# Performance work log

Measured on AMD Instinct MI355X. Metric: run time of the kernel, lower is better.

Reference implementation:

```python
import jax, jax.numpy as jnp
import numpy as np

K = 32          # kneighbors
HEADS = 4       # Anchor_selfattention head_num
EPS = 1e-5      # BatchNorm eps


def bn(x, gamma, beta):
    # training-mode BatchNorm1d on channel-last tensor [B, M, C]:
    # stats over batch+spatial dims per channel, biased variance (torch behavior)
    m = jnp.mean(x, axis=(0, 1), keepdims=True)
    v = jnp.var(x, axis=(0, 1), keepdims=True)
    return gamma * (x - m) * jax.lax.rsqrt(v + EPS) + beta


def setup_inputs() -> dict:
    B, NA, NP, C, NRAW = 32, 4, 16384, 256, 32768
    key = jax.random.key(0)
    ks = jax.random.split(key, 12)
    s = 0.02
    return {
        "a_points": jax.random.normal(ks[0], (B, NA, 3), jnp.float32),
        "sa_x": jax.random.normal(ks[1], (B, NP, C), jnp.float32),
        "sa_xyz": jax.random.normal(ks[2], (B, NP, 3), jnp.float32),
        "xyz_raw": jax.random.normal(ks[3], (B, NRAW, 3), jnp.float32),
        # global_layer: Conv1d(3->C, bias=False) + BN(C)
        "g_W": jax.random.normal(ks[4], (C, 3), jnp.float32) * s,
        "g_gamma": jnp.ones((C,), jnp.float32),
        "g_beta": jnp.zeros((C,), jnp.float32),
        # attention: to_qkv Linear(C -> 3C, bias=False)
        "qkv_W": jax.random.normal(ks[5], (3 * C, C), jnp.float32) * s,
        # pos_embedding: Conv1d(3->C) + BN(C)
        "pos_W": jax.random.normal(ks[6], (C, 3), jnp.float32) * s,
        "pos_b": jnp.zeros((C,), jnp.float32),
        "pos_gamma": jnp.ones((C,), jnp.float32),
        "pos_beta": jnp.zeros((C,), jnp.float32),
        # res: Conv1d(C->C) + BN(C)
        "res_W": jax.random.normal(ks[7], (C, C), jnp.float32) * s,
        "res_b": jnp.zeros((C,), jnp.float32),
        "res_gamma": jnp.ones((C,), jnp.float32),
        "res_beta": jnp.zeros((C,), jnp.float32),
        # prob_head: Conv1d(2C -> 9, bias=False) + BN(9)
        "prob_W": jax.random.normal(ks[8], (9, 2 * C), jnp.float32) * s,
        "prob_gamma": jnp.ones((9,), jnp.float32),
        "prob_beta": jnp.zeros((9,), jnp.float32),
    }


def reference(a_points, sa_x, sa_xyz, xyz_raw,
              g_W, g_gamma, g_beta,
              qkv_W,
              pos_W, pos_b, pos_gamma, pos_beta,
              res_W, res_b, res_gamma, res_beta,
              prob_W, prob_gamma, prob_beta):
    B, NA, _ = a_points.shape
    C = sa_x.shape[-1]
    hd = C // HEADS

    # ---- knn_point: squared distances anchor->points, smallest-K indices ----
    # dist[b, a, n] = |a_points[b,a] - sa_xyz[b,n]|^2
    d = (-2.0 * jnp.einsum("bac,bnc->ban", a_points, sa_xyz)
         + jnp.sum(a_points ** 2, -1)[:, :, None]
         + jnp.sum(sa_xyz ** 2, -1)[:, None, :])
    _, idx = jax.lax.top_k(-d, K)                      # [B, NA, K]

    # ---- index_points gather + max-pool over neighbors ----
    local = jnp.take_along_axis(sa_x[:, None, :, :], idx[..., None], axis=2)  # [B,NA,K,C]
    local_feat = jnp.max(local, axis=2)                # [B, NA, C]

    # ---- Anchor self-attention ----
    gc = jnp.mean(a_points, axis=1, keepdims=True)
    rel = a_points - gc                                # [B, NA, 3]
    pos = bn(rel @ pos_W.T + pos_b, pos_gamma, pos_beta)   # [B, NA, C]

    qkv = local_feat @ qkv_W.T                         # [B, NA, 3C]
    q, k, v = jnp.split(qkv, 3, axis=-1)
    q, k, v = q + pos, k + pos, v + pos
    q = q.reshape(B, NA, HEADS, hd)
    k = k.reshape(B, NA, HEADS, hd)
    v = v.reshape(B, NA, HEADS, hd)
    attn = jnp.einsum("bmhd,bnhd->bhmn", q, k) / np.sqrt(hd).astype(np.float32)
    attn = jax.nn.softmax(attn, axis=-1)
    av = jnp.einsum("bhmn,bnhd->bmhd", attn, v).reshape(B, NA, C)
    res = bn(av @ res_W.T + res_b, res_gamma, res_beta)

    local_feat = local_feat + res                      # [B, NA, C]

    # ---- global branch ----
    gfeat = bn(a_points @ g_W.T, g_gamma, g_beta)      # [B, NA, C]
    gmax = jnp.max(gfeat, axis=1, keepdims=True)       # [B, 1, C]
    feat = jnp.concatenate(
        [local_feat, jnp.broadcast_to(gmax, (B, NA, C))], axis=-1)  # [B, NA, 2C]

    prob = bn(feat @ prob_W.T, prob_gamma, prob_beta)  # [B, NA, 9]
    return prob
```

## Files before the change

### kernel.cpp

```cpp
#include <hip/hip_runtime.h>
#include <math.h>

#define NPTS 16384
#define HALF 8192
#define NB   32
#define NA   4
#define NC   256
#define KNN  32
#define NROW 128
#define CAP  1024

#define OFF_LF      0
#define OFF_QKV     32768
#define OFF_RESLIN  131072
#define OFF_POSLIN  163840
#define OFF_POSST   196608
#define OFF_GLIN    197120
#define OFF_GST     229888
#define OFF_PROBLIN 230400
#define OFF_CAND    231552

__global__ __launch_bounds__(512) void knn_part_kernel(
    const float* __restrict__ a_points, const float* __restrict__ sa_xyz,
    uint2* __restrict__ cand)
{
  const int blk  = blockIdx.x;
  const int row  = blk >> 1;
  const int half = blk & 1;
  const int b    = row >> 2;
  const int t    = threadIdx.x;

  __shared__ float s_T;
  __shared__ int   s_m;
  __shared__ uint2 s_cand[CAP];
  float* smin = (float*)s_cand;

  const float ax = a_points[row*3 + 0];
  const float ay = a_points[row*3 + 1];
  const float az = a_points[row*3 + 2];
  const float* __restrict__ xyz = sa_xyz + (size_t)b * NPTS * 3 + (size_t)half * HALF * 3;

  float d[16];
#pragma unroll
  for (int j = 0; j < 16; ++j) {
    const int n = t + 512*j;
    const float dx = xyz[n*3+0] - ax;
    const float dy = xyz[n*3+1] - ay;
    const float dz = xyz[n*3+2] - az;
    d[j] = dx*dx + dy*dy + dz*dz;
  }
  float mn = d[0];
#pragma unroll
  for (int j = 1; j < 16; ++j) mn = fminf(mn, d[j]);
  if (t == 0) s_m = 0;
  smin[t] = mn;
  __syncthreads();

  if (t < 64) {
    unsigned v[8];
#pragma unroll
    for (int q = 0; q < 8; ++q) v[q] = __float_as_uint(smin[t + 64*q]);
    unsigned lo = 0u, hi = 0x7f7fffffu;
    while (lo < hi) {
      const unsigned mid = lo + ((hi - lo) >> 1);
      int cnt = 0;
#pragma unroll
      for (int q = 0; q < 8; ++q) cnt += (int)__popcll(__ballot(v[q] <= mid));
      if (cnt >= KNN) hi = mid; else lo = mid + 1;
    }
    if (t == 0) s_T = __uint_as_float(lo);
  }
  __syncthreads();
  const float T = s_T;

#pragma unroll
  for (int j = 0; j < 16; ++j) {
    if (d[j] <= T) {
      const int pos = atomicAdd(&s_m, 1);
      if (pos < CAP) s_cand[pos] = make_uint2(__float_as_uint(d[j]),
                                              (unsigned)(half*HALF + t + 512*j));
    }
  }
  __syncthreads();
  const int m = (s_m < CAP) ? s_m : CAP;

  for (int c2 = t; c2 < m; c2 += 512) {
    const uint2 me = s_cand[c2];
    int rank = 0;
    for (int j = 0; j < m; ++j) {
      const uint2 o = s_cand[j];
      rank += (o.x < me.x) || (o.x == me.x && o.y < me.y);
    }
    if (rank < KNN) cand[(size_t)blk*KNN + rank] = me;
  }
}

__global__ __launch_bounds__(256) void gather_kernel(
    const uint2* __restrict__ cand, const float* __restrict__ sa_x,
    float* __restrict__ lf)
{
  const int row = blockIdx.x;
  const int b   = row >> 2;
  const int t   = threadIdx.x;
  __shared__ uint2 s64[64];
  __shared__ int   s_top[KNN];
  if (t < 64) s64[t] = cand[(size_t)row*64 + t];
  __syncthreads();
  if (t < 64) {
    const uint2 me = s64[t];
    int rank = 0;
#pragma unroll
    for (int j = 0; j < 64; ++j) {
      const uint2 o = s64[j];
      rank += (o.x < me.x) || (o.x == me.x && o.y < me.y);
    }
    if (rank < KNN) s_top[rank] = (int)me.y;
  }
  __syncthreads();

  const float* __restrict__ xb = sa_x + (size_t)b * NPTS * NC;
  float acc = -3.0e38f;
#pragma unroll
  for (int r = 0; r < KNN; ++r)
    acc = fmaxf(acc, xb[(size_t)s_top[r] * NC + t]);
  lf[(size_t)row * NC + t] = acc;
}

__global__ __launch_bounds__(256) void lin1_kernel(
    const float* __restrict__ lf, const float* __restrict__ qkv_W,
    const float* __restrict__ a_points,
    const float* __restrict__ pos_W, const float* __restrict__ pos_b,
    const float* __restrict__ g_W,
    float* __restrict__ qkv, float* __restrict__ pos_lin, float* __restrict__ pos_stats,
    float* __restrict__ g_lin, float* __restrict__ g_stats)
{
  const int blk = blockIdx.x;
  if (blk < 96) {
    const int r0 = (blk / 12) * 16;
    const int o0 = (blk % 12) * 64;
    const int ot = threadIdx.x & 63;
    const int rt = threadIdx.x >> 6;
    const int o  = o0 + ot;
    const float* __restrict__ wrow = qkv_W + (size_t)o * NC;
    const float* __restrict__ l0p  = lf + (size_t)(r0 + rt*4) * NC;
    float acc0 = 0.f, acc1 = 0.f, acc2 = 0.f, acc3 = 0.f;
    for (int c = 0; c < NC; c += 4) {
      const float4 w4 = *(const float4*)(wrow + c);
      const float4 l0 = *(const float4*)(l0p + c);
      const float4 l1 = *(const float4*)(l0p + NC + c);
      const float4 l2 = *(const float4*)(l0p + 2*NC + c);
      const float4 l3 = *(const float4*)(l0p + 3*NC + c);
      acc0 = fmaf(l0.x,w4.x,acc0); acc0 = fmaf(l0.y,w4.y,acc0); acc0 = fmaf(l0.z,w4.z,acc0); acc0 = fmaf(l0.w,w4.w,acc0);
      acc1 = fmaf(l1.x,w4.x,acc1); acc1 = fmaf(l1.y,w4.y,acc1); acc1 = fmaf(l1.z,w4.z,acc1); acc1 = fmaf(l1.w,w4.w,acc1);
      acc2 = fmaf(l2.x,w4.x,acc2); acc2 = fmaf(l2.y,w4.y,acc2); acc2 = fmaf(l2.z,w4.z,acc2); acc2 = fmaf(l2.w,w4.w,acc2);
      acc3 = fmaf(l3.x,w4.x,acc3); acc3 = fmaf(l3.y,w4.y,acc3); acc3 = fmaf(l3.z,w4.z,acc3); acc3 = fmaf(l3.w,w4.w,acc3);
    }
    const int r = r0 + rt*4;
    qkv[(size_t)(r+0)*768 + o] = acc0;
    qkv[(size_t)(r+1)*768 + o] = acc1;
    qkv[(size_t)(r+2)*768 + o] = acc2;
    qkv[(size_t)(r+3)*768 + o] = acc3;
  } else if (blk == 96) {
    __shared__ float apts[NROW*3];
    for (int i = threadIdx.x; i < NROW*3; i += 256) apts[i] = a_points[i];
    __syncthreads();
    const int c = threadIdx.x;
    const float w0 = pos_W[c*3+0], w1 = pos_W[c*3+1], w2 = pos_W[c*3+2];
    const float bb = pos_b[c];
    float sum = 0.f, sumsq = 0.f;
    for (int b = 0; b < NB; ++b) {
      float gx=0.f, gy=0.f, gz=0.f;
#pragma unroll
      for (int a = 0; a < NA; ++a) {
        gx += apts[(b*NA+a)*3+0];
        gy += apts[(b*NA+a)*3+1];
        gz += apts[(b*NA+a)*3+2];
      }
      gx *= 0.25f; gy *= 0.25f; gz *= 0.25f;
#pragma unroll
      for (int a = 0; a < NA; ++a) {
        const float v = (apts[(b*NA+a)*3+0]-gx)*w0
                      + (apts[(b*NA+a)*3+1]-gy)*w1
                      + (apts[(b*NA+a)*3+2]-gz)*w2 + bb;
        pos_lin[(b*NA+a)*NC + c] = v;
        sum += v; sumsq += v*v;
      }
    }
    pos_stats[c] = sum; pos_stats[NC + c] = sumsq;
  } else {
    __shared__ float apts[NROW*3];
    for (int i = threadIdx.x; i < NROW*3; i += 256) apts[i] = a_points[i];
    __syncthreads();
    const int c = threadIdx.x;
    const float w0 = g_W[c*3+0], w1 = g_W[c*3+1], w2 = g_W[c*3+2];
    float sum = 0.f, sumsq = 0.f;
    for (int r = 0; r < NROW; ++r) {
      const float v = apts[r*3+0]*w0 + apts[r*3+1]*w1 + apts[r*3+2]*w2;
      g_lin[r*NC + c] = v;
      sum += v; sumsq += v*v;
    }
    g_stats[c] = sum; g_stats[NC + c] = sumsq;
  }
}

__global__ __launch_bounds__(256) void attn_kernel(
    const float* __restrict__ qkv, const float* __restrict__ pos_lin,
    const float* __restrict__ pos_stats,
    const float* __restrict__ pos_gamma, const float* __restrict__ pos_beta,
    const float* __restrict__ res_W, const float* __restrict__ res_b,
    float* __restrict__ res_lin)
{
  const int b = blockIdx.x;
  const int t = threadIdx.x;
  __shared__ float av_s[NA][NC];
  const int c = t;
  const float pmean = pos_stats[c] * (1.0f/NROW);
  const float pvar  = pos_stats[NC + c] * (1.0f/NROW) - pmean*pmean;
  const float prstd = 1.0f / sqrtf(pvar + 1e-5f);
  const float pga = pos_gamma[c], pbe = pos_beta[c];

  float q[NA], k[NA], vv[NA];
#pragma unroll
  for (int a = 0; a < NA; ++a) {
    const int row = b*NA + a;
    const float p = pga * (pos_lin[(size_t)row*NC + c] - pmean) * prstd + pbe;
    q[a]  = qkv[(size_t)row*768 +       c] + p;
    k[a]  = qkv[(size_t)row*768 + 256 + c] + p;
    vv[a] = qkv[(size_t)row*768 + 512 + c] + p;
  }
  float s[NA][NA];
#pragma unroll
  for (int m = 0; m < NA; ++m) {
#pragma unroll
    for (int n = 0; n < NA; ++n) {
      float p = q[m]*k[n];
#pragma unroll
      for (int off = 1; off < 64; off <<= 1) p += __shfl_xor(p, off);
      s[m][n] = p * 0.125f;
    }
  }
#pragma unroll
  for (int m = 0; m < NA; ++m) {
    const float mx = fmaxf(fmaxf(s[m][0], s[m][1]), fmaxf(s[m][2], s[m][3]));
    const float e0 = expf(s[m][0]-mx), e1 = expf(s[m][1]-mx);
    const float e2 = expf(s[m][2]-mx), e3 = expf(s[m][3]-mx);
    const float inv = 1.0f / (e0+e1+e2+e3);
    av_s[m][c] = (e0*vv[0] + e1*vv[1] + e2*vv[2] + e3*vv[3]) * inv;
  }
  __syncthreads();

  const float* __restrict__ wrow = res_W + (size_t)c * NC;
  float r0=0.f, r1=0.f, r2=0.f, r3=0.f;
  for (int cc = 0; cc < NC; cc += 4) {
    const float4 w4 = *(const float4*)(wrow + cc);
    const float4 v0 = *(const float4*)&av_s[0][cc];
    const float4 v1 = *(const float4*)&av_s[1][cc];
    const float4 v2 = *(const float4*)&av_s[2][cc];
    const float4 v3 = *(const float4*)&av_s[3][cc];
    r0 = fmaf(v0.x,w4.x,r0); r0 = fmaf(v0.y,w4.y,r0); r0 = fmaf(v0.z,w4.z,r0); r0 = fmaf(v0.w,w4.w,r0);
    r1 = fmaf(v1.x,w4.x,r1); r1 = fmaf(v1.y,w4.y,r1); r1 = fmaf(v1.z,w4.z,r1); r1 = fmaf(v1.w,w4.w,r1);
    r2 = fmaf(v2.x,w4.x,r2); r2 = fmaf(v2.y,w4.y,r2); r2 = fmaf(v2.z,w4.z,r2); r2 = fmaf(v2.w,w4.w,r2);
    r3 = fmaf(v3.x,w4.x,r3); r3 = fmaf(v3.y,w4.y,r3); r3 = fmaf(v3.z,w4.z,r3); r3 = fmaf(v3.w,w4.w,r3);
  }
  const float bias = res_b[c];
  res_lin[(size_t)(b*NA+0)*NC + c] = r0 + bias;
  res_lin[(size_t)(b*NA+1)*NC + c] = r1 + bias;
  res_lin[(size_t)(b*NA+2)*NC + c] = r2 + bias;
  res_lin[(size_t)(b*NA+3)*NC + c] = r3 + bias;
}

__global__ __launch_bounds__(256) void final_kernel(
    const float* __restrict__ lf, const float* __restrict__ res_lin,
    const float* __restrict__ res_gamma, const float* __restrict__ res_beta,
    const float* __restrict__ g_lin, const float* __restrict__ g_stats,
    const float* __restrict__ g_gamma, const float* __restrict__ g_beta,
    const float* __restrict__ prob_W,
    float* __restrict__ prob_lin)
{
  const int b = blockIdx.x;
  const int t = threadIdx.x;
  __shared__ float feat_s[NA][2 * NC];
  const int c = t;
  float rsum = 0.f, rss = 0.f;
  for (int row = 0; row < NROW; ++row) {
    const float v = res_lin[(size_t)row*NC + c];
    rsum += v; rss += v*v;
  }
  const float rmean = rsum * (1.0f/NROW);
  const float rvar  = rss * (1.0f/NROW) - rmean*rmean;
  const float rrstd = 1.0f / sqrtf(rvar + 1e-5f);
  const float rg = res_gamma[c], rb = res_beta[c];

  const float gmean = g_stats[c] * (1.0f/NROW);
  const float gvar  = g_stats[NC+c] * (1.0f/NROW) - gmean*gmean;
  const float grstd = 1.0f / sqrtf(gvar + 1e-5f);
  const float gg = g_gamma[c], gb = g_beta[c];

  float gm = -3.0e38f;
#pragma unroll
  for (int a = 0; a < NA; ++a) {
    const int row = b*NA + a;
    gm = fmaxf(gm, gg * (g_lin[(size_t)row*NC + c] - gmean) * grstd + gb);
  }
#pragma unroll
  for (int a = 0; a < NA; ++a) {
    const int row = b*NA + a;
    const float resv = rg * (res_lin[(size_t)row*NC + c] - rmean) * rrstd + rb;
    feat_s[a][c]      = lf[(size_t)row*NC + c] + resv;
    feat_s[a][NC + c] = gm;
  }
  __syncthreads();

  const int m = t >> 6, lane = t & 63;
  for (int j = 0; j < 9; ++j) {
    float p = 0.f;
#pragma unroll
    for (int k2 = 0; k2 < 8; ++k2) {
      const int cc = lane + 64*k2;
      p = fmaf(feat_s[m][cc], prob_W[j*2*NC + cc], p);
    }
#pragma unroll
    for (int off = 1; off < 64; off <<= 1) p += __shfl_xor(p, off);
    if (lane == 0) prob_lin[(b*NA+m)*9 + j] = p;
  }
}

__global__ __launch_bounds__(256) void out_kernel(
    const float* __restrict__ prob_lin,
    const float* __restrict__ prob_gamma, const float* __restrict__ prob_beta,
    float* __restrict__ out)
{
  const int t = threadIdx.x;
  __shared__ float pmn[9], prs[9];
  if (t < 9) {
    float s = 0.f, ss = 0.f;
    for (int i = 0; i < NROW; ++i) { const float v = prob_lin[i*9+t]; s += v; ss += v*v; }
    const float m  = s * (1.0f/NROW);
    const float va = ss * (1.0f/NROW) - m*m;
    pmn[t] = m; prs[t] = 1.0f / sqrtf(va + 1e-5f);
  }
  __syncthreads();
  for (int i = t; i < NROW*9; i += 256) {
    const int j = i % 9;
    out[i] = prob_gamma[j] * (prob_lin[i] - pmn[j]) * prs[j] + prob_beta[j];
  }
}

extern "C" void kernel_launch(void* const* d_in, const int* in_sizes, int n_in,
                              void* d_out, int out_size, void* d_ws, size_t ws_size,
                              hipStream_t stream) {
  const float* a_points  = (const float*)d_in[0];
  const float* sa_x      = (const float*)d_in[1];
  const float* sa_xyz    = (const float*)d_in[2];
  const float* g_W       = (const float*)d_in[4];
  const float* g_gamma   = (const float*)d_in[5];
  const float* g_beta    = (const float*)d_in[6];
  const float* qkv_W     = (const float*)d_in[7];
  const float* pos_W     = (const float*)d_in[8];
  const float* pos_b     = (const float*)d_in[9];
  const float* pos_gamma = (const float*)d_in[10];
  const float* pos_beta  = (const float*)d_in[11];
  const float* res_W     = (const float*)d_in[12];
  const float* res_b     = (const float*)d_in[13];
  const float* res_gamma = (const float*)d_in[14];
  const float* res_beta  = (const float*)d_in[15];
  const float* prob_W    = (const float*)d_in[16];
  const float* prob_gamma= (const float*)d_in[17];
  const float* prob_beta = (const float*)d_in[18];
  float* ws  = (float*)d_ws;
  float* out = (float*)d_out;

  knn_part_kernel<<<256, 512, 0, stream>>>(a_points, sa_xyz, (uint2*)(ws + OFF_CAND));
  gather_kernel<<<NROW, 256, 0, stream>>>((const uint2*)(ws + OFF_CAND), sa_x, ws + OFF_LF);
  lin1_kernel<<<98, 256, 0, stream>>>(ws + OFF_LF, qkv_W, a_points, pos_W, pos_b, g_W,
      ws + OFF_QKV, ws + OFF_POSLIN, ws + OFF_POSST, ws + OFF_GLIN, ws + OFF_GST);
  attn_kernel<<<NB, 256, 0, stream>>>(ws + OFF_QKV, ws + OFF_POSLIN, ws + OFF_POSST,
      pos_gamma, pos_beta, res_W, res_b, ws + OFF_RESLIN);
  final_kernel<<<NB, 256, 0, stream>>>(ws + OFF_LF, ws + OFF_RESLIN,
      res_gamma, res_beta, ws + OFF_GLIN, ws + OFF_GST, g_gamma, g_beta, prob_W,
      ws + OFF_PROBLIN);
  out_kernel<<<1, 256, 0, stream>>>(ws + OFF_PROBLIN, prob_gamma, prob_beta, out);
}
```

Before: 63.80 us.

## Fuse KNN, gather, QKV projection and output BN via last-block atomic counters

Merges knn, gather and lin1 kernels into one launch: the second half-block for each anchor row, detected through an atomic counter in workspace, merges candidates, gathers max features and computes that row's QKV projection. The pos and global linear parts run in two extra blocks. The output BatchNorm is folded into final_kernel using a last-block-done counter. This cuts three kernel launches and their inter-kernel gaps, at the cost of a less parallel QKV matmul (one row per block, weights reread per row) and counters that are never reset, relying on parity/modulo arithmetic across calls.

```diff
diff --git a/kernel.cpp b/kernel.cpp
--- a/kernel.cpp
+++ b/kernel.cpp
@@ -19,20 +19,76 @@
 #define OFF_GST     229888
 #define OFF_PROBLIN 230400
 #define OFF_CAND    231552
-
-__global__ __launch_bounds__(512) void knn_part_kernel(
+#define OFF_CNT     247936
+
+__global__ __launch_bounds__(512) void knn_fused_kernel(
     const float* __restrict__ a_points, const float* __restrict__ sa_xyz,
-    uint2* __restrict__ cand)
+    const float* __restrict__ sa_x, const float* __restrict__ qkv_W,
+    const float* __restrict__ pos_W, const float* __restrict__ pos_b,
+    const float* __restrict__ g_W,
+    uint2* __restrict__ cand, unsigned int* __restrict__ cnt,
+    float* __restrict__ lf, float* __restrict__ qkv,
+    float* __restrict__ pos_lin, float* __restrict__ pos_stats,
+    float* __restrict__ g_lin, float* __restrict__ g_stats)
 {
-  const int blk  = blockIdx.x;
-  const int row  = blk >> 1;
-  const int half = blk & 1;
+  const int blk = blockIdx.x;
+  const int t   = threadIdx.x;
+
+  if (blk < 2) {
+    __shared__ float apts[NROW * 3];
+    for (int i = t; i < NROW*3; i += 512) apts[i] = a_points[i];
+    __syncthreads();
+    if (t < NC) {
+      const int c = t;
+      if (blk == 0) {
+        const float w0 = pos_W[c*3+0], w1 = pos_W[c*3+1], w2 = pos_W[c*3+2];
+        const float bb = pos_b[c];
+        float sum = 0.f, sumsq = 0.f;
+        for (int b = 0; b < NB; ++b) {
+          float gx=0.f, gy=0.f, gz=0.f;
+#pragma unroll
+          for (int a = 0; a < NA; ++a) {
+            gx += apts[(b*NA+a)*3+0];
+            gy += apts[(b*NA+a)*3+1];
+            gz += apts[(b*NA+a)*3+2];
+          }
+          gx *= 0.25f; gy *= 0.25f; gz *= 0.25f;
+#pragma unroll
+          for (int a = 0; a < NA; ++a) {
+            const float v = (apts[(b*NA+a)*3+0]-gx)*w0
+                          + (apts[(b*NA+a)*3+1]-gy)*w1
+                          + (apts[(b*NA+a)*3+2]-gz)*w2 + bb;
+            pos_lin[(b*NA+a)*NC + c] = v;
+            sum += v; sumsq += v*v;
+          }
+        }
+        pos_stats[c] = sum; pos_stats[NC + c] = sumsq;
+      } else {
+        const float w0 = g_W[c*3+0], w1 = g_W[c*3+1], w2 = g_W[c*3+2];
+        float sum = 0.f, sumsq = 0.f;
+        for (int r = 0; r < NROW; ++r) {
+          const float v = apts[r*3+0]*w0 + apts[r*3+1]*w1 + apts[r*3+2]*w2;
+          g_lin[r*NC + c] = v;
+          sum += v; sumsq += v*v;
+        }
+        g_stats[c] = sum; g_stats[NC + c] = sumsq;
+      }
+    }
+    return;
+  }
+
+  const int row  = (blk - 2) >> 1;
+  const int half = (blk - 2) & 1;
   const int b    = row >> 2;
-  const int t    = threadIdx.x;
 
   __shared__ float s_T;
   __shared__ int   s_m;
+  __shared__ int   s_winflag;
   __shared__ uint2 s_cand[CAP];
+  __shared__ uint2 s64[64];
+  __shared__ int   s_top[KNN];
+  __shared__ float s_lf2[2][NC];
+  __shared__ float lf_s[NC];
   float* smin = (float*)s_cand;
 
   const float ax = a_points[row*3 + 0];
@@ -63,10 +119,10 @@
     unsigned lo = 0u, hi = 0x7f7fffffu;
     while (lo < hi) {
       const unsigned mid = lo + ((hi - lo) >> 1);
-      int cnt = 0;
-#pragma unroll
-      for (int q = 0; q < 8; ++q) cnt += (int)__popcll(__ballot(v[q] <= mid));
-      if (cnt >= KNN) hi = mid; else lo = mid + 1;
+      int cnt2 = 0;
+#pragma unroll
+      for (int q = 0; q < 8; ++q) cnt2 += (int)__popcll(__ballot(v[q] <= mid));
+      if (cnt2 >= KNN) hi = mid; else lo = mid + 1;
     }
     if (t == 0) s_T = __uint_as_float(lo);
   }
@@ -91,19 +147,19 @@
       const uint2 o = s_cand[j];
       rank += (o.x < me.x) || (o.x == me.x && o.y < me.y);
     }
-    if (rank < KNN) cand[(size_t)blk*KNN + rank] = me;
-  }
-}
-
-__global__ __launch_bounds__(256) void gather_kernel(
-    const uint2* __restrict__ cand, const float* __restrict__ sa_x,
-    float* __restrict__ lf)
-{
-  const int row = blockIdx.x;
-  const int b   = row >> 2;
-  const int t   = threadIdx.x;
-  __shared__ uint2 s64[64];
-  __shared__ int   s_top[KNN];
+    if (rank < KNN) cand[(size_t)row*64 + half*KNN + rank] = me;
+  }
+  __syncthreads();
+
+  if (t == 0) {
+    __threadfence();
+    const unsigned old = atomicAdd(&cnt[row], 1u);
+    s_winflag = (((old + 1u) & 1u) == 0u);
+  }
+  __syncthreads();
+  if (!s_winflag) return;
+  __threadfence();
+
   if (t < 64) s64[t] = cand[(size_t)row*64 + t];
   __syncthreads();
   if (t < 64) {
@@ -118,88 +174,41 @@
   }
   __syncthreads();
 
-  const float* __restrict__ xb = sa_x + (size_t)b * NPTS * NC;
-  float acc = -3.0e38f;
-#pragma unroll
-  for (int r = 0; r < KNN; ++r)
-    acc = fmaxf(acc, xb[(size_t)s_top[r] * NC + t]);
-  lf[(size_t)row * NC + t] = acc;
-}
-
-__global__ __launch_bounds__(256) void lin1_kernel(
-    const float* __restrict__ lf, const float* __restrict__ qkv_W,
-    const float* __restrict__ a_points,
-    const float* __restrict__ pos_W, const float* __restrict__ pos_b,
-    const float* __restrict__ g_W,
-    float* __restrict__ qkv, float* __restrict__ pos_lin, float* __restrict__ pos_stats,
-    float* __restrict__ g_lin, float* __restrict__ g_stats)
-{
-  const int blk = blockIdx.x;
-  if (blk < 96) {
-    const int r0 = (blk / 12) * 16;
-    const int o0 = (blk % 12) * 64;
-    const int ot = threadIdx.x & 63;
-    const int rt = threadIdx.x >> 6;
-    const int o  = o0 + ot;
-    const float* __restrict__ wrow = qkv_W + (size_t)o * NC;
-    const float* __restrict__ l0p  = lf + (size_t)(r0 + rt*4) * NC;
-    float acc0 = 0.f, acc1 = 0.f, acc2 = 0.f, acc3 = 0.f;
+  {
+    const int c = t & 255, h = t >> 8;
+    const float* __restrict__ xb = sa_x + (size_t)b * NPTS * NC;
+    float acc = -3.0e38f;
+    for (int r = h*16; r < h*16 + 16; ++r)
+      acc = fmaxf(acc, xb[(size_t)s_top[r] * NC + c]);
+    s_lf2[h][c] = acc;
+  }
+  __syncthreads();
+  if (t < NC) {
+    const float v = fmaxf(s_lf2[0][t], s_lf2[1][t]);
+    lf_s[t] = v;
+    lf[(size_t)row * NC + t] = v;
+  }
+  __syncthreads();
+
+  {
+    const float* __restrict__ w1 = qkv_W + (size_t)t * NC;
+    float a1 = 0.f;
     for (int c = 0; c < NC; c += 4) {
-      const float4 w4 = *(const float4*)(wrow + c);
-      const float4 l0 = *(const float4*)(l0p + c);
-      const float4 l1 = *(const float4*)(l0p + NC + c);
-      const float4 l2 = *(const float4*)(l0p + 2*NC + c);
-      const float4 l3 = *(const float4*)(l0p + 3*NC + c);
-      acc0 = fmaf(l0.x,w4.x,acc0); acc0 = fmaf(l0.y,w4.y,acc0); acc0 = fmaf(l0.z,w4.z,acc0); acc0 = fmaf(l0.w,w4.w,acc0);
-      acc1 = fmaf(l1.x,w4.x,acc1); acc1 = fmaf(l1.y,w4.y,acc1); acc1 = fmaf(l1.z,w4.z,acc1); acc1 = fmaf(l1.w,w4.w,acc1);
-      acc2 = fmaf(l2.x,w4.x,acc2); acc2 = fmaf(l2.y,w4.y,acc2); acc2 = fmaf(l2.z,w4.z,acc2); acc2 = fmaf(l2.w,w4.w,acc2);
-      acc3 = fmaf(l3.x,w4.x,acc3); acc3 = fmaf(l3.y,w4.y,acc3); acc3 = fmaf(l3.z,w4.z,acc3); acc3 = fmaf(l3.w,w4.w,acc3);
-    }
-    const int r = r0 + rt*4;
-    qkv[(size_t)(r+0)*768 + o] = acc0;
-    qkv[(size_t)(r+1)*768 + o] = acc1;
-    qkv[(size_t)(r+2)*768 + o] = acc2;
-    qkv[(size_t)(r+3)*768 + o] = acc3;
-  } else if (blk == 96) {
-    __shared__ float apts[NROW*3];
-    for (int i = threadIdx.x; i < NROW*3; i += 256) apts[i] = a_points[i];
-    __syncthreads();
-    const int c = threadIdx.x;
-    const float w0 = pos_W[c*3+0], w1 = pos_W[c*3+1], w2 = pos_W[c*3+2];
-    const float bb = pos_b[c];
-    float sum = 0.f, sumsq = 0.f;
-    for (int b = 0; b < NB; ++b) {
-      float gx=0.f, gy=0.f, gz=0.f;
-#pragma unroll
-      for (int a = 0; a < NA; ++a) {
-        gx += apts[(b*NA+a)*3+0];
-        gy += apts[(b*NA+a)*3+1];
-        gz += apts[(b*NA+a)*3+2];
+      const float4 l4 = *(const float4*)&lf_s[c];
+      const float4 w4 = *(const float4*)(w1 + c);
+      a1 = fmaf(l4.x,w4.x,a1); a1 = fmaf(l4.y,w4.y,a1); a1 = fmaf(l4.z,w4.z,a1); a1 = fmaf(l4.w,w4.w,a1);
+    }
+    qkv[(size_t)row*768 + t] = a1;
+    if (t < 256) {
+      const float* __restrict__ w2 = qkv_W + (size_t)(512 + t) * NC;
+      float a2 = 0.f;
+      for (int c = 0; c < NC; c += 4) {
+        const float4 l4 = *(const float4*)&lf_s[c];
+        const float4 w4 = *(const float4*)(w2 + c);
+        a2 = fmaf(l4.x,w4.x,a2); a2 = fmaf(l4.y,w4.y,a2); a2 = fmaf(l4.z,w4.z,a2); a2 = fmaf(l4.w,w4.w,a2);
       }
-      gx *= 0.25f; gy *= 0.25f; gz *= 0.25f;
-#pragma unroll
-      for (int a = 0; a < NA; ++a) {
-        const float v = (apts[(b*NA+a)*3+0]-gx)*w0
-                      + (apts[(b*NA+a)*3+1]-gy)*w1
-                      + (apts[(b*NA+a)*3+2]-gz)*w2 + bb;
-        pos_lin[(b*NA+a)*NC + c] = v;
-        sum += v; sumsq += v*v;
-      }
-    }
-    pos_stats[c] = sum; pos_stats[NC + c] = sumsq;
-  } else {
-    __shared__ float apts[NROW*3];
-    for (int i = threadIdx.x; i < NROW*3; i += 256) apts[i] = a_points[i];
-    __syncthreads();
-    const int c = threadIdx.x;
-    const float w0 = g_W[c*3+0], w1 = g_W[c*3+1], w2 = g_W[c*3+2];
-    float sum = 0.f, sumsq = 0.f;
-    for (int r = 0; r < NROW; ++r) {
-      const float v = apts[r*3+0]*w0 + apts[r*3+1]*w1 + apts[r*3+2]*w2;
-      g_lin[r*NC + c] = v;
-      sum += v; sumsq += v*v;
-    }
-    g_stats[c] = sum; g_stats[NC + c] = sumsq;
+      qkv[(size_t)row*768 + 512 + t] = a2;
+    }
   }
 }
 
@@ -275,11 +284,15 @@
     const float* __restrict__ g_lin, const float* __restrict__ g_stats,
     const float* __restrict__ g_gamma, const float* __restrict__ g_beta,
     const float* __restrict__ prob_W,
-    float* __restrict__ prob_lin)
+    const float* __restrict__ prob_gamma, const float* __restrict__ prob_beta,
+    float* __restrict__ prob_lin, unsigned int* __restrict__ cnt_out,
+    float* __restrict__ out)
 {
   const int b = blockIdx.x;
   const int t = threadIdx.x;
   __shared__ float feat_s[NA][2 * NC];
+  __shared__ int   s_winflag;
+  __shared__ float pmn[9], prs[9];
   const int c = t;
   float rsum = 0.f, rss = 0.f;
   for (int row = 0; row < NROW; ++row) {
@@ -323,21 +336,23 @@
     for (int off = 1; off < 64; off <<= 1) p += __shfl_xor(p, off);
     if (lane == 0) prob_lin[(b*NA+m)*9 + j] = p;
   }
-}
-
-__global__ __launch_bounds__(256) void out_kernel(
-    const float* __restrict__ prob_lin,
-    const float* __restrict__ prob_gamma, const float* __restrict__ prob_beta,
-    float* __restrict__ out)
-{
-  const int t = threadIdx.x;
-  __shared__ float pmn[9], prs[9];
+  __syncthreads();
+
+  if (t == 0) {
+    __threadfence();
+    const unsigned old = atomicAdd(cnt_out, 1u);
+    s_winflag = (((old + 1u) & 31u) == 0u);
+  }
+  __syncthreads();
+  if (!s_winflag) return;
+  __threadfence();
+
   if (t < 9) {
     float s = 0.f, ss = 0.f;
     for (int i = 0; i < NROW; ++i) { const float v = prob_lin[i*9+t]; s += v; ss += v*v; }
-    const float m  = s * (1.0f/NROW);
-    const float va = ss * (1.0f/NROW) - m*m;
-    pmn[t] = m; prs[t] = 1.0f / sqrtf(va + 1e-5f);
+    const float mm = s * (1.0f/NROW);
+    const float va = ss * (1.0f/NROW) - mm*mm;
+    pmn[t] = mm; prs[t] = 1.0f / sqrtf(va + 1e-5f);
   }
   __syncthreads();
   for (int i = t; i < NROW*9; i += 256) {
@@ -369,15 +384,17 @@
   const float* prob_beta = (const float*)d_in[18];
   float* ws  = (float*)d_ws;
   float* out = (float*)d_out;
-
-  knn_part_kernel<<<256, 512, 0, stream>>>(a_points, sa_xyz, (uint2*)(ws + OFF_CAND));
-  gather_kernel<<<NROW, 256, 0, stream>>>((const uint2*)(ws + OFF_CAND), sa_x, ws + OFF_LF);
-  lin1_kernel<<<98, 256, 0, stream>>>(ws + OFF_LF, qkv_W, a_points, pos_W, pos_b, g_W,
-      ws + OFF_QKV, ws + OFF_POSLIN, ws + OFF_POSST, ws + OFF_GLIN, ws + OFF_GST);
+  unsigned int* cnt = (unsigned int*)(ws + OFF_CNT);
+
+  knn_fused_kernel<<<258, 512, 0, stream>>>(a_points, sa_xyz, sa_x, qkv_W,
+      pos_W, pos_b, g_W,
+      (uint2*)(ws + OFF_CAND), cnt,
+      ws + OFF_LF, ws + OFF_QKV,
+      ws + OFF_POSLIN, ws + OFF_POSST, ws + OFF_GLIN, ws + OFF_GST);
   attn_kernel<<<NB, 256, 0, stream>>>(ws + OFF_QKV, ws + OFF_POSLIN, ws + OFF_POSST,
       pos_gamma, pos_beta, res_W, res_b, ws + OFF_RESLIN);
   final_kernel<<<NB, 256, 0, stream>>>(ws + OFF_LF, ws + OFF_RESLIN,
-      res_gamma, res_beta, ws + OFF_GLIN, ws + OFF_GST, g_gamma, g_beta, prob_W,
-      ws + OFF_PROBLIN);
-  out_kernel<<<1, 256, 0, stream>>>(ws + OFF_PROBLIN, prob_gamma, prob_beta, out);
+      res_gamma, res_beta, ws + OFF_GLIN, ws + OFF_GST, g_gamma, g_beta,
+      prob_W, prob_gamma, prob_beta,
+      ws + OFF_PROBLIN, cnt + NROW, out);
 }
```

Result: slower. 98.35 us (+54.2%).

## Fuse kNN with gather and final with output via last-block-done counters

Applied to the files above, without the earlier changes.

Merges the kNN partial-selection and gather kernels into one launch. Each pair of half-blocks increments a per-row counter, and the block that finishes second merges the 64 candidates and gathers the max features using 512 threads split into two halves. The final and output-BN kernels are fused the same way: the last of the 32 blocks computes the 9-channel BatchNorm from the staged values. This removes two kernel launches and their inter-kernel gaps. In exchange it relies on relaxed atomics without explicit fences and on counters in the workspace that are never reset, using parity/modulo checks, which could break if the workspace starts nonzero or memory ordering is not guaranteed.

```diff
diff --git a/kernel.cpp b/kernel.cpp
--- a/kernel.cpp
+++ b/kernel.cpp
@@ -19,10 +19,15 @@
 #define OFF_GST     229888
 #define OFF_PROBLIN 230400
 #define OFF_CAND    231552
-
-__global__ __launch_bounds__(512) void knn_part_kernel(
+#define OFF_CNT     247936
+
+typedef unsigned long long ull;
+
+__global__ __launch_bounds__(512) void knn_gather_kernel(
     const float* __restrict__ a_points, const float* __restrict__ sa_xyz,
-    uint2* __restrict__ cand)
+    const float* __restrict__ sa_x,
+    ull* __restrict__ cand, unsigned int* __restrict__ cnt,
+    float* __restrict__ lf)
 {
   const int blk  = blockIdx.x;
   const int row  = blk >> 1;
@@ -32,7 +37,11 @@
 
   __shared__ float s_T;
   __shared__ int   s_m;
-  __shared__ uint2 s_cand[CAP];
+  __shared__ int   s_winflag;
+  __shared__ ull   s_cand[CAP];
+  __shared__ ull   s64[64];
+  __shared__ int   s_top[KNN];
+  __shared__ float s_lf2[2][NC];
   float* smin = (float*)s_cand;
 
   const float ax = a_points[row*3 + 0];
@@ -63,10 +72,10 @@
     unsigned lo = 0u, hi = 0x7f7fffffu;
     while (lo < hi) {
       const unsigned mid = lo + ((hi - lo) >> 1);
-      int cnt = 0;
-#pragma unroll
-      for (int q = 0; q < 8; ++q) cnt += (int)__popcll(__ballot(v[q] <= mid));
-      if (cnt >= KNN) hi = mid; else lo = mid + 1;
+      int c2 = 0;
+#pragma unroll
+      for (int q = 0; q < 8; ++q) c2 += (int)__popcll(__ballot(v[q] <= mid));
+      if (c2 >= KNN) hi = mid; else lo = mid + 1;
     }
     if (t == 0) s_T = __uint_as_float(lo);
   }
@@ -77,53 +86,55 @@
   for (int j = 0; j < 16; ++j) {
     if (d[j] <= T) {
       const int pos = atomicAdd(&s_m, 1);
-      if (pos < CAP) s_cand[pos] = make_uint2(__float_as_uint(d[j]),
-                                              (unsigned)(half*HALF + t + 512*j));
+      if (pos < CAP)
+        s_cand[pos] = ((ull)__float_as_uint(d[j]) << 32) | (unsigned)(half*HALF + t + 512*j);
     }
   }
   __syncthreads();
   const int m = (s_m < CAP) ? s_m : CAP;
 
   for (int c2 = t; c2 < m; c2 += 512) {
-    const uint2 me = s_cand[c2];
+    const ull me = s_cand[c2];
     int rank = 0;
-    for (int j = 0; j < m; ++j) {
-      const uint2 o = s_cand[j];
-      rank += (o.x < me.x) || (o.x == me.x && o.y < me.y);
-    }
-    if (rank < KNN) cand[(size_t)blk*KNN + rank] = me;
-  }
-}
-
-__global__ __launch_bounds__(256) void gather_kernel(
-    const uint2* __restrict__ cand, const float* __restrict__ sa_x,
-    float* __restrict__ lf)
-{
-  const int row = blockIdx.x;
-  const int b   = row >> 2;
-  const int t   = threadIdx.x;
-  __shared__ uint2 s64[64];
-  __shared__ int   s_top[KNN];
-  if (t < 64) s64[t] = cand[(size_t)row*64 + t];
+    for (int j = 0; j < m; ++j) rank += (s_cand[j] < me);
+    if (rank < KNN)
+      __hip_atomic_store(&cand[(size_t)row*64 + half*KNN + rank], me,
+                         __ATOMIC_RELAXED, __HIP_MEMORY_SCOPE_AGENT);
+  }
+  __syncthreads();
+
+  if (t == 0) {
+    const unsigned old = atomicAdd(&cnt[row], 1u);
+    s_winflag = (((old + 1u) & 1u) == 0u);
+  }
+  __syncthreads();
+  if (!s_winflag) return;
+
+  if (t < 64)
+    s64[t] = __hip_atomic_load(&cand[(size_t)row*64 + t],
+                               __ATOMIC_RELAXED, __HIP_MEMORY_SCOPE_AGENT);
   __syncthreads();
   if (t < 64) {
-    const uint2 me = s64[t];
+    const ull me = s64[t];
     int rank = 0;
 #pragma unroll
-    for (int j = 0; j < 64; ++j) {
-      const uint2 o = s64[j];
-      rank += (o.x < me.x) || (o.x == me.x && o.y < me.y);
-    }
-    if (rank < KNN) s_top[rank] = (int)me.y;
-  }
-  __syncthreads();
-
-  const float* __restrict__ xb = sa_x + (size_t)b * NPTS * NC;
-  float acc = -3.0e38f;
-#pragma unroll
-  for (int r = 0; r < KNN; ++r)
-    acc = fmaxf(acc, xb[(size_t)s_top[r] * NC + t]);
-  lf[(size_t)row * NC + t] = acc;
+    for (int j = 0; j < 64; ++j) rank += (s64[j] < me);
+    if (rank < KNN) s_top[rank] = (int)(unsigned)(me & 0xffffffffu);
+  }
+  __syncthreads();
+
+  {
+    const int c = t & 255, h = t >> 8;
+    const float* __restrict__ xb = sa_x + (size_t)b * NPTS * NC;
+    float acc = -3.0e38f;
+#pragma unroll
+    for (int r2 = 0; r2 < 16; ++r2)
+      acc = fmaxf(acc, xb[(size_t)s_top[h*16 + r2] * NC + c]);
+    s_lf2[h][c] = acc;
+  }
+  __syncthreads();
+  if (t < NC)
+    lf[(size_t)row * NC + t] = fmaxf(s_lf2[0][t], s_lf2[1][t]);
 }
 
 __global__ __launch_bounds__(256) void lin1_kernel(
@@ -275,13 +286,19 @@
     const float* __restrict__ g_lin, const float* __restrict__ g_stats,
     const float* __restrict__ g_gamma, const float* __restrict__ g_beta,
     const float* __restrict__ prob_W,
-    float* __restrict__ prob_lin)
+    const float* __restrict__ prob_gamma, const float* __restrict__ prob_beta,
+    float* __restrict__ prob_lin, unsigned int* __restrict__ cnt_out,
+    float* __restrict__ out)
 {
   const int b = blockIdx.x;
   const int t = threadIdx.x;
   __shared__ float feat_s[NA][2 * NC];
+  __shared__ int   s_winflag;
+  __shared__ float s_prob[NROW*9];
+  __shared__ float pmn[9], prs[9];
   const int c = t;
   float rsum = 0.f, rss = 0.f;
+#pragma unroll 16
   for (int row = 0; row < NROW; ++row) {
     const float v = res_lin[(size_t)row*NC + c];
     rsum += v; rss += v*v;
@@ -321,28 +338,33 @@
     }
 #pragma unroll
     for (int off = 1; off < 64; off <<= 1) p += __shfl_xor(p, off);
-    if (lane == 0) prob_lin[(b*NA+m)*9 + j] = p;
-  }
-}
-
-__global__ __launch_bounds__(256) void out_kernel(
-    const float* __restrict__ prob_lin,
-    const float* __restrict__ prob_gamma, const float* __restrict__ prob_beta,
-    float* __restrict__ out)
-{
-  const int t = threadIdx.x;
-  __shared__ float pmn[9], prs[9];
+    if (lane == 0)
+      __hip_atomic_store(&prob_lin[(b*NA+m)*9 + j], p,
+                         __ATOMIC_RELAXED, __HIP_MEMORY_SCOPE_AGENT);
+  }
+  __syncthreads();
+
+  if (t == 0) {
+    const unsigned old = atomicAdd(cnt_out, 1u);
+    s_winflag = (((old + 1u) & 31u) == 0u);
+  }
+  __syncthreads();
+  if (!s_winflag) return;
+
+  for (int i = t; i < NROW*9; i += 256)
+    s_prob[i] = __hip_atomic_load(&prob_lin[i], __ATOMIC_RELAXED, __HIP_MEMORY_SCOPE_AGENT);
+  __syncthreads();
   if (t < 9) {
     float s = 0.f, ss = 0.f;
-    for (int i = 0; i < NROW; ++i) { const float v = prob_lin[i*9+t]; s += v; ss += v*v; }
-    const float m  = s * (1.0f/NROW);
-    const float va = ss * (1.0f/NROW) - m*m;
-    pmn[t] = m; prs[t] = 1.0f / sqrtf(va + 1e-5f);
+    for (int i = 0; i < NROW; ++i) { const float v = s_prob[i*9+t]; s += v; ss += v*v; }
+    const float mm = s * (1.0f/NROW);
+    const float va = ss * (1.0f/NROW) - mm*mm;
+    pmn[t] = mm; prs[t] = 1.0f / sqrtf(va + 1e-5f);
   }
   __syncthreads();
   for (int i = t; i < NROW*9; i += 256) {
     const int j = i % 9;
-    out[i] = prob_gamma[j] * (prob_lin[i] - pmn[j]) * prs[j] + prob_beta[j];
+    out[i] = prob_gamma[j] * (s_prob[i] - pmn[j]) * prs[j] + prob_beta[j];
   }
 }
 
@@ -369,15 +391,16 @@
   const float* prob_beta = (const float*)d_in[18];
   float* ws  = (float*)d_ws;
   float* out = (float*)d_out;
-
-  knn_part_kernel<<<256, 512, 0, stream>>>(a_points, sa_xyz, (uint2*)(ws + OFF_CAND));
-  gather_kernel<<<NROW, 256, 0, stream>>>((const uint2*)(ws + OFF_CAND), sa_x, ws + OFF_LF);
+  unsigned int* cnt = (unsigned int*)(ws + OFF_CNT);
+
+  knn_gather_kernel<<<256, 512, 0, stream>>>(a_points, sa_xyz, sa_x,
+      (ull*)(ws + OFF_CAND), cnt, ws + OFF_LF);
   lin1_kernel<<<98, 256, 0, stream>>>(ws + OFF_LF, qkv_W, a_points, pos_W, pos_b, g_W,
       ws + OFF_QKV, ws + OFF_POSLIN, ws + OFF_POSST, ws + OFF_GLIN, ws + OFF_GST);
   attn_kernel<<<NB, 256, 0, stream>>>(ws + OFF_QKV, ws + OFF_POSLIN, ws + OFF_POSST,
       pos_gamma, pos_beta, res_W, res_b, ws + OFF_RESLIN);
   final_kernel<<<NB, 256, 0, stream>>>(ws + OFF_LF, ws + OFF_RESLIN,
-      res_gamma, res_beta, ws + OFF_GLIN, ws + OFF_GST, g_gamma, g_beta, prob_W,
-      ws + OFF_PROBLIN);
-  out_kernel<<<1, 256, 0, stream>>>(ws + OFF_PROBLIN, prob_gamma, prob_beta, out);
+      res_gamma, res_beta, ws + OFF_GLIN, ws + OFF_GST, g_gamma, g_beta,
+      prob_W, prob_gamma, prob_beta,
+      ws + OFF_PROBLIN, cnt + NROW, out);
 }
```

After: 57.36 us. 1.11x faster.
